# Optimization experiments

Hardware: AMD Instinct MI355X
Metric: run time of the kernel (lower is better)

## Reference

```python
import jax, jax.numpy as jnp
import numpy as np

N = 50000
E = 1600000
SI, SO, VI, VO, H, SVOD = 128, 128, 16, 16, 16, 3
EPS = 1e-8


def _safe_norm(x, axis, keepdims=False):
    return jnp.sqrt(jnp.sum(x * x, axis=axis, keepdims=keepdims) + EPS)


def setup_inputs() -> dict:
    key = jax.random.key(0)
    ks = jax.random.split(key, 13)

    def lin(k, fan_in, shape):
        b = 1.0 / np.sqrt(fan_in)
        return jax.random.uniform(k, shape, jnp.float32, -b, b)

    merged_dim = H + SI + 3 * SVOD  # 153
    return {
        "s": jax.random.normal(ks[0], (N, SI), jnp.float32),
        "v": jax.random.normal(ks[1], (N, VI, 3), jnp.float32),
        "frames": jax.random.normal(ks[2], (E, 3, 3), jnp.float32),
        "W_vd": lin(ks[3], VI, (VI, H)),            # vector_down (no bias)
        "W_vdf": lin(ks[4], VI, (VI, SVOD)),        # vector_down_frames (no bias)
        "W_so": lin(ks[5], merged_dim, (merged_dim, SO)),  # scalar_out
        "b_so": lin(ks[6], merged_dim, (SO,)),
        "W_vu": lin(ks[7], H, (H, VO)),             # vector_up (no bias)
        "W_vosf": lin(ks[8], SO, (SO, 3 * SVOD)),   # vector_out_scale_frames
        "b_vosf": lin(ks[9], SO, (3 * SVOD,)),
        "W_vuf": lin(ks[10], SVOD, (SVOD, VO)),     # vector_up_frames (no bias)
        "edge_index": jax.random.randint(ks[11], (2, E), 0, N, jnp.int32),
        "node_inputs": 1,
    }


def reference(s, v, frames, W_vd, W_vdf, W_so, b_so, W_vu, W_vosf, b_vosf, W_vuf, edge_index, node_inputs):
    # node_inputs is assumed truthy (node-wise GCP): gather by source node, scatter-mean back.
    row = edge_index[0]
    deg = jax.ops.segment_sum(jnp.ones((E,), s.dtype), row, num_segments=N)
    inv_deg = 1.0 / jnp.maximum(deg, 1.0)

    v_pre = jnp.swapaxes(v, -1, -2)                 # [N, 3, VI]
    vh = v_pre @ W_vd                                # [N, 3, H]
    vnorm = _safe_norm(vh, axis=-2)                  # [N, H]
    vdf = v_pre @ W_vdf                              # [N, 3, SVOD]

    # scalarize: project gathered source-node vectors onto per-edge frames, scatter-mean
    local = jnp.einsum('eij,ejc->eic', frames, vdf[row])       # [E, 3, SVOD]
    local9 = jnp.swapaxes(local, -1, -2).reshape(E, 3 * SVOD)  # [E, 9]
    sh = jax.ops.segment_sum(local9, row, num_segments=N) * inv_deg[:, None]  # [N, 9]

    merged = jnp.concatenate([s, vnorm, sh], axis=-1)          # [N, SI+H+9]
    scalar_rep = merged @ W_so + b_so                           # [N, SO]

    # vector path with frame gate
    vr = jnp.swapaxes(vh @ W_vu, -1, -2)                        # [N, VO, 3]
    gate = jax.nn.sigmoid(scalar_rep) @ W_vosf + b_vosf         # [N, 9]
    # vectorize: expand gate scalars back into vectors via frames, scatter-mean
    g = gate[row].reshape(E, 3, 3)
    gv_e = jnp.einsum('eji,ejk->eik', g, frames)                # [E, 3, 3]
    gv = jax.ops.segment_sum(gv_e, row, num_segments=N) * inv_deg[:, None, None]  # [N, 3, 3]
    gvr = jnp.swapaxes(jnp.swapaxes(gv, -1, -2) @ W_vuf, -1, -2)  # [N, VO, 3]
    vr = vr * jax.nn.sigmoid(_safe_norm(gvr, axis=-1, keepdims=True))

    return jax.nn.relu(scalar_rep), vr
```

## Files before the change

kernel.cpp:

```cpp
#include <hip/hip_runtime.h>

#define N_NODES 50000
#define N_EDGES 1600000
#define NPB     16
#define NCHAIN  16
#define MSTR    164
#define EPSV    1e-8f

typedef float f32x4 __attribute__((ext_vector_type(4)));
typedef short s16x8 __attribute__((ext_vector_type(8)));

__device__ __forceinline__ float sigmoidf_(float x) { return 1.0f / (1.0f + __expf(-x)); }
__device__ __forceinline__ short f2bf(float x) {
    unsigned u = __float_as_uint(x);
    unsigned r = (u + 0x7FFFu + ((u >> 16) & 1u)) >> 16;
    return (short)r;
}
__device__ __forceinline__ float bf2f(short h) {
    return __uint_as_float(((unsigned)(unsigned short)h) << 16);
}

__global__ __launch_bounds__(256) void prep_w_kernel(
    const float* __restrict__ W_so, short* __restrict__ Whi, short* __restrict__ Wlo) {
    int i = blockIdx.x * 256 + threadIdx.x;
    if (i >= 160 * 128) return;
    int k = i >> 7;
    float w = (k < 153) ? W_so[i] : 0.0f;
    short hh = f2bf(w);
    Whi[i] = hh;
    Wlo[i] = f2bf(w - bf2f(hh));
}

__global__ __launch_bounds__(256) void bucket_kernel(
    const int* __restrict__ row,
    int* __restrict__ head,
    int* __restrict__ nxt) {
    int e = blockIdx.x * 256 + threadIdx.x;
    if (e >= N_EDGES) return;
    int r = row[e];
    int prev = atomicExch(&head[r * NCHAIN + (e & (NCHAIN - 1))], e);
    nxt[e] = prev;
}

__global__ __launch_bounds__(256) void node_kernel(
    const float* __restrict__ s,
    const float* __restrict__ v,
    const float* __restrict__ frames,
    const float* __restrict__ W_vd,
    const float* __restrict__ W_vdf,
    const short* __restrict__ Whi,
    const short* __restrict__ Wlo,
    const float* __restrict__ b_so,
    const float* __restrict__ W_vu,
    const float* __restrict__ W_vosf,
    const float* __restrict__ b_vosf,
    const float* __restrict__ W_vuf,
    const int* __restrict__ head,
    const int* __restrict__ nxt,
    float* __restrict__ out0,
    float* __restrict__ out1)
{
    __shared__ float vL[NPB][48];
    __shared__ float vhL[NPB][3][16];
    __shared__ __align__(16) float mergedL[NPB][MSTR];
    __shared__ float redL[NPB][16][11];
    __shared__ float tmpL[NPB][10];
    __shared__ float FbarL[NPB][9];
    __shared__ float vdfL[NPB][9];
    __shared__ __align__(16) float sigL[NPB][128];
    __shared__ float gateL[NPB][12];

    const int t = threadIdx.x;
    const int base = blockIdx.x * NPB;
    const int nn = t >> 4, h = t & 15;
    const int n = base + nn;

#pragma unroll
    for (int r = 0; r < 3; r++) vL[nn][h * 3 + r] = v[(size_t)n * 48 + h * 3 + r];
#pragma unroll
    for (int r = 0; r < 8; r++) mergedL[nn][h * 8 + r] = s[(size_t)n * 128 + h * 8 + r];

    {
        float fs[10];
#pragma unroll
        for (int k = 0; k < 10; k++) fs[k] = 0.f;
        int e = head[(size_t)n * NCHAIN + h];
        while (e >= 0) {
            int en = nxt[e];
            const float* f = frames + (size_t)e * 9;
#pragma unroll
            for (int k = 0; k < 9; k++) fs[k] += f[k];
            fs[9] += 1.0f;
            e = en;
        }
#pragma unroll
        for (int k = 0; k < 10; k++) redL[nn][h][k] = fs[k];
    }
    __syncthreads();

    if (h < 10) {
        float a = 0.f;
#pragma unroll
        for (int j = 0; j < 16; j++) a += redL[nn][j][h];
        tmpL[nn][h] = a;
    }
    __syncthreads();

    {
        float vh0 = 0.f, vh1 = 0.f, vh2 = 0.f;
#pragma unroll
        for (int i = 0; i < 16; i++) {
            float w = W_vd[i * 16 + h];
            vh0 += vL[nn][i * 3 + 0] * w;
            vh1 += vL[nn][i * 3 + 1] * w;
            vh2 += vL[nn][i * 3 + 2] * w;
        }
        vhL[nn][0][h] = vh0; vhL[nn][1][h] = vh1; vhL[nn][2][h] = vh2;
        mergedL[nn][128 + h] = sqrtf(vh0 * vh0 + vh1 * vh1 + vh2 * vh2 + EPSV);
        if (h < 9) {
            float inv = 1.0f / fmaxf(tmpL[nn][9], 1.0f);
            FbarL[nn][h] = tmpL[nn][h] * inv;
        }
        if (h < 3) {
            int cc = h;
#pragma unroll
            for (int j = 0; j < 3; j++) {
                float a = 0.f;
#pragma unroll
                for (int i = 0; i < 16; i++) a += vL[nn][i * 3 + j] * W_vdf[i * 3 + cc];
                vdfL[nn][j * 3 + cc] = a;
            }
        }
    }
    __syncthreads();

    {
        if (h < 9) {
            int c = h / 3, i = h % 3;
            float a = 0.f;
#pragma unroll
            for (int j = 0; j < 3; j++) a += FbarL[nn][i * 3 + j] * vdfL[nn][j * 3 + c];
            mergedL[nn][144 + h] = a;
        } else {
            mergedL[nn][144 + h] = 0.0f;
        }
        if (h < 4) mergedL[nn][160 + h] = 0.0f;
    }
    __syncthreads();

    {
        const int w = t >> 6;
        const int lane = t & 63;
        const int quad = lane >> 4;
        const int col = lane & 15;
        f32x4 acc[2];
        acc[0] = (f32x4){0.f, 0.f, 0.f, 0.f};
        acc[1] = (f32x4){0.f, 0.f, 0.f, 0.f};
#pragma unroll
        for (int kk = 0; kk < 5; kk++) {
            const int krow = kk * 32 + quad * 8;
            const float* ap = &mergedL[col][krow];
            float4 a0v = *(const float4*)ap;
            float4 a1v = *(const float4*)(ap + 4);
            float av[8] = {a0v.x, a0v.y, a0v.z, a0v.w, a1v.x, a1v.y, a1v.z, a1v.w};
            s16x8 ahi, alo;
#pragma unroll
            for (int j = 0; j < 8; j++) {
                short hh = f2bf(av[j]);
                ahi[j] = hh;
                alo[j] = f2bf(av[j] - bf2f(hh));
            }
#pragma unroll
            for (int t0 = 0; t0 < 2; t0++) {
                int o = w * 32 + t0 * 16 + col;
                s16x8 bhi, blo;
#pragma unroll
                for (int j = 0; j < 8; j++) {
                    bhi[j] = Whi[(krow + j) * 128 + o];
                    blo[j] = Wlo[(krow + j) * 128 + o];
                }
                acc[t0] = __builtin_amdgcn_mfma_f32_16x16x32_bf16(ahi, bhi, acc[t0], 0, 0, 0);
                acc[t0] = __builtin_amdgcn_mfma_f32_16x16x32_bf16(ahi, blo, acc[t0], 0, 0, 0);
                acc[t0] = __builtin_amdgcn_mfma_f32_16x16x32_bf16(alo, bhi, acc[t0], 0, 0, 0);
            }
        }
#pragma unroll
        for (int t0 = 0; t0 < 2; t0++) {
            int o = w * 32 + t0 * 16 + col;
            float bso = b_so[o];
#pragma unroll
            for (int r = 0; r < 4; r++) {
                int nl = quad * 4 + r;
                float val = acc[t0][r] + bso;
                out0[(size_t)(base + nl) * 128 + o] = fmaxf(val, 0.0f);
                sigL[nl][o] = sigmoidf_(val);
            }
        }
    }
    __syncthreads();

    {
        const float* sp = &sigL[nn][h * 8];
        float4 s0 = *(const float4*)sp;
        float4 s1 = *(const float4*)(sp + 4);
        float sv[8] = {s0.x, s0.y, s0.z, s0.w, s1.x, s1.y, s1.z, s1.w};
        float p[9];
#pragma unroll
        for (int k = 0; k < 9; k++) p[k] = 0.f;
#pragma unroll
        for (int i = 0; i < 8; i++) {
            int o = h * 8 + i;
#pragma unroll
            for (int k = 0; k < 9; k++) p[k] += sv[i] * W_vosf[o * 9 + k];
        }
#pragma unroll
        for (int k = 0; k < 9; k++) redL[nn][h][k] = p[k];
    }
    __syncthreads();
    if (h < 9) {
        float a = b_vosf[h];
#pragma unroll
        for (int j = 0; j < 16; j++) a += redL[nn][j][h];
        gateL[nn][h] = a;
    }
    __syncthreads();

    {
        int o = h;
        float gv[9];
#pragma unroll
        for (int i = 0; i < 3; i++)
#pragma unroll
            for (int kk = 0; kk < 3; kk++) {
                float a = 0.f;
#pragma unroll
                for (int j = 0; j < 3; j++) a += gateL[nn][j * 3 + i] * FbarL[nn][j * 3 + kk];
                gv[i * 3 + kk] = a;
            }
        float gvr[3];
#pragma unroll
        for (int kk = 0; kk < 3; kk++) {
            float a = 0.f;
#pragma unroll
            for (int i = 0; i < 3; i++) a += gv[i * 3 + kk] * W_vuf[i * 16 + o];
            gvr[kk] = a;
        }
        float gn2 = sqrtf(gvr[0] * gvr[0] + gvr[1] * gvr[1] + gvr[2] * gvr[2] + EPSV);
        float sg = sigmoidf_(gn2);
#pragma unroll
        for (int c = 0; c < 3; c++) {
            float a = 0.f;
#pragma unroll
            for (int h2 = 0; h2 < 16; h2++) a += vhL[nn][c][h2] * W_vu[h2 * 16 + o];
            out1[(size_t)n * 48 + o * 3 + c] = a * sg;
        }
    }
}

extern "C" void kernel_launch(void* const* d_in, const int* in_sizes, int n_in,
                              void* d_out, int out_size, void* d_ws, size_t ws_size,
                              hipStream_t stream) {
    const float* s      = (const float*)d_in[0];
    const float* v      = (const float*)d_in[1];
    const float* frames = (const float*)d_in[2];
    const float* W_vd   = (const float*)d_in[3];
    const float* W_vdf  = (const float*)d_in[4];
    const float* W_so   = (const float*)d_in[5];
    const float* b_so   = (const float*)d_in[6];
    const float* W_vu   = (const float*)d_in[7];
    const float* W_vosf = (const float*)d_in[8];
    const float* b_vosf = (const float*)d_in[9];
    const float* W_vuf  = (const float*)d_in[10];
    const int* edge_index = (const int*)d_in[11];

    const size_t head_b = (size_t)N_NODES * NCHAIN * sizeof(int);
    const size_t next_b = (size_t)N_EDGES * sizeof(int);
    int*   head = (int*)d_ws;
    int*   nxt  = (int*)((char*)d_ws + head_b);
    short* Whi  = (short*)((char*)d_ws + head_b + next_b);
    short* Wlo  = Whi + 160 * 128;
    float* out0 = (float*)d_out;
    float* out1 = out0 + (size_t)N_NODES * 128;

    hipMemsetAsync(head, 0xFF, head_b, stream);
    prep_w_kernel<<<(160 * 128 + 255) / 256, 256, 0, stream>>>(W_so, Whi, Wlo);
    bucket_kernel<<<(N_EDGES + 255) / 256, 256, 0, stream>>>(edge_index, head, nxt);
    node_kernel<<<N_NODES / NPB, 256, 0, stream>>>(
        s, v, frames, W_vd, W_vdf, Whi, Wlo, b_so, W_vu, W_vosf, b_vosf, W_vuf,
        head, nxt, out0, out1);
}
```

Measured before the change: 291.3 us.

## Shrink node kernel LDS with aliasing and shuffle reductions, raise occupancy

```diff
diff --git a/kernel.cpp b/kernel.cpp
--- a/kernel.cpp
+++ b/kernel.cpp
@@ -42,7 +42,7 @@
     nxt[e] = prev;
 }
 
-__global__ __launch_bounds__(256) void node_kernel(
+__global__ __launch_bounds__(256, 8) void node_kernel(
     const float* __restrict__ s,
     const float* __restrict__ v,
     const float* __restrict__ frames,
@@ -60,31 +60,31 @@
     float* __restrict__ out0,
     float* __restrict__ out1)
 {
+    __shared__ __align__(16) float poolL[NPB][MSTR];
     __shared__ float vL[NPB][48];
     __shared__ float vhL[NPB][3][16];
-    __shared__ __align__(16) float mergedL[NPB][MSTR];
-    __shared__ float redL[NPB][16][11];
-    __shared__ float tmpL[NPB][10];
     __shared__ float FbarL[NPB][9];
     __shared__ float vdfL[NPB][9];
-    __shared__ __align__(16) float sigL[NPB][128];
     __shared__ float gateL[NPB][12];
+
+    float (*sigL)[128] = (float (*)[128])&poolL[0][0];
 
     const int t = threadIdx.x;
     const int base = blockIdx.x * NPB;
     const int nn = t >> 4, h = t & 15;
     const int n = base + nn;
 
+    int e = head[(size_t)n * NCHAIN + h];
+
 #pragma unroll
     for (int r = 0; r < 3; r++) vL[nn][h * 3 + r] = v[(size_t)n * 48 + h * 3 + r];
 #pragma unroll
-    for (int r = 0; r < 8; r++) mergedL[nn][h * 8 + r] = s[(size_t)n * 128 + h * 8 + r];
+    for (int r = 0; r < 8; r++) poolL[nn][h * 8 + r] = s[(size_t)n * 128 + h * 8 + r];
 
     {
         float fs[10];
 #pragma unroll
         for (int k = 0; k < 10; k++) fs[k] = 0.f;
-        int e = head[(size_t)n * NCHAIN + h];
         while (e >= 0) {
             int en = nxt[e];
             const float* f = frames + (size_t)e * 9;
@@ -94,15 +94,14 @@
             e = en;
         }
 #pragma unroll
-        for (int k = 0; k < 10; k++) redL[nn][h][k] = fs[k];
-    }
-    __syncthreads();
-
-    if (h < 10) {
-        float a = 0.f;
-#pragma unroll
-        for (int j = 0; j < 16; j++) a += redL[nn][j][h];
-        tmpL[nn][h] = a;
+        for (int m = 1; m < 16; m <<= 1) {
+#pragma unroll
+            for (int k = 0; k < 10; k++) fs[k] += __shfl_xor(fs[k], m);
+        }
+        if (h < 9) {
+            float inv = 1.0f / fmaxf(fs[9], 1.0f);
+            FbarL[nn][h] = fs[h] * inv;
+        }
     }
     __syncthreads();
 
@@ -116,11 +115,7 @@
             vh2 += vL[nn][i * 3 + 2] * w;
         }
         vhL[nn][0][h] = vh0; vhL[nn][1][h] = vh1; vhL[nn][2][h] = vh2;
-        mergedL[nn][128 + h] = sqrtf(vh0 * vh0 + vh1 * vh1 + vh2 * vh2 + EPSV);
-        if (h < 9) {
-            float inv = 1.0f / fmaxf(tmpL[nn][9], 1.0f);
-            FbarL[nn][h] = tmpL[nn][h] * inv;
-        }
+        poolL[nn][128 + h] = sqrtf(vh0 * vh0 + vh1 * vh1 + vh2 * vh2 + EPSV);
         if (h < 3) {
             int cc = h;
 #pragma unroll
@@ -140,11 +135,11 @@
             float a = 0.f;
 #pragma unroll
             for (int j = 0; j < 3; j++) a += FbarL[nn][i * 3 + j] * vdfL[nn][j * 3 + c];
-            mergedL[nn][144 + h] = a;
+            poolL[nn][144 + h] = a;
         } else {
-            mergedL[nn][144 + h] = 0.0f;
-        }
-        if (h < 4) mergedL[nn][160 + h] = 0.0f;
+            poolL[nn][144 + h] = 0.0f;
+        }
+        if (h < 4) poolL[nn][160 + h] = 0.0f;
     }
     __syncthreads();
 
@@ -159,7 +154,7 @@
 #pragma unroll
         for (int kk = 0; kk < 5; kk++) {
             const int krow = kk * 32 + quad * 8;
-            const float* ap = &mergedL[col][krow];
+            const float* ap = &poolL[col][krow];
             float4 a0v = *(const float4*)ap;
             float4 a1v = *(const float4*)(ap + 4);
             float av[8] = {a0v.x, a0v.y, a0v.z, a0v.w, a1v.x, a1v.y, a1v.z, a1v.w};
@@ -184,6 +179,7 @@
                 acc[t0] = __builtin_amdgcn_mfma_f32_16x16x32_bf16(alo, bhi, acc[t0], 0, 0, 0);
             }
         }
+        __syncthreads();
 #pragma unroll
         for (int t0 = 0; t0 < 2; t0++) {
             int o = w * 32 + t0 * 16 + col;
@@ -214,14 +210,11 @@
             for (int k = 0; k < 9; k++) p[k] += sv[i] * W_vosf[o * 9 + k];
         }
 #pragma unroll
-        for (int k = 0; k < 9; k++) redL[nn][h][k] = p[k];
-    }
-    __syncthreads();
-    if (h < 9) {
-        float a = b_vosf[h];
-#pragma unroll
-        for (int j = 0; j < 16; j++) a += redL[nn][j][h];
-        gateL[nn][h] = a;
+        for (int m = 1; m < 16; m <<= 1) {
+#pragma unroll
+            for (int k = 0; k < 9; k++) p[k] += __shfl_xor(p[k], m);
+        }
+        if (h < 9) gateL[nn][h] = p[h] + b_vosf[h];
     }
     __syncthreads();
 
```

After: 305.2 us. +4.8%, slower.
